# Kernel tuning notes

Hardware: AMD Instinct MI355X
Metric: run time of the kernel (lower is better)

Reference implementation:

```python
import jax, jax.numpy as jnp
import numpy as np

B, IN_LEN, NN, IN_DIM = 32, 28, 2048, 1
E, ND = 256, 256          # embed_dim, node_dim
H = E + ND                # hidden_dim = 512
N_LAYERS = 3
OUT_LEN = 28


def setup_inputs() -> dict:
    key = jax.random.key(0)
    ks = jax.random.split(key, 16)
    x_node = jax.random.normal(ks[0], (B, IN_LEN, NN, IN_DIM), jnp.float32)
    # x_state channels: [0]=cumulative cases, [1]=infected I, [2]=population N
    col0 = jax.random.uniform(ks[1], (B, IN_LEN, NN, 1), jnp.float32) * 100.0
    colI = jax.random.uniform(ks[2], (B, IN_LEN, NN, 1), jnp.float32) * 100.0 + 1.0
    colN = 1e4 * (1.0 + 0.1 * jax.random.uniform(ks[3], (B, IN_LEN, NN, 1), jnp.float32))
    x_state = jnp.concatenate([col0, colI, colN], axis=-1)
    node_emb = jax.random.normal(ks[4], (NN, ND), jnp.float32) * 0.05
    W_ts = jax.random.normal(ks[5], (E, IN_DIM * IN_LEN), jnp.float32) * 0.05
    b_ts = jnp.zeros((E,), jnp.float32)
    enc_W1 = jax.random.normal(ks[6], (N_LAYERS, H, H), jnp.float32) * 0.02
    enc_b1 = jnp.zeros((N_LAYERS, H), jnp.float32)
    enc_W2 = jax.random.normal(ks[7], (N_LAYERS, H, H), jnp.float32) * 0.02
    enc_b2 = jnp.zeros((N_LAYERS, H), jnp.float32)
    Wb = jax.random.normal(ks[8], (1, H), jnp.float32) * 0.05
    bb = jnp.zeros((1,), jnp.float32)
    Wg = jax.random.normal(ks[9], (1, H), jnp.float32) * 0.05
    bg = jnp.zeros((1,), jnp.float32)
    return dict(x_node=x_node, x_state=x_state, node_emb=node_emb,
                W_ts=W_ts, b_ts=b_ts, enc_W1=enc_W1, enc_b1=enc_b1,
                enc_W2=enc_W2, enc_b2=enc_b2, Wb=Wb, bb=bb, Wg=Wg, bg=bg)


def _forward(x_node, x_state, node_emb, W_ts, b_ts,
             enc_W1, enc_b1, enc_W2, enc_b2, Wb, bb, Wg, bg):
    Bn, Lh, Nn, _ = x_node.shape
    # [B,L,N,D] -> [B,N,L*D] (channel = in_dim*in_len for 1x1 conv == linear)
    flat = jnp.transpose(x_node[..., :IN_DIM], (0, 2, 1, 3)).reshape(Bn, Nn, Lh * IN_DIM)
    ts = flat @ W_ts.T + b_ts                                  # [B,N,E]
    h = jnp.concatenate(
        [ts, jnp.broadcast_to(node_emb[None], (Bn,) + node_emb.shape)], axis=-1)  # [B,N,H]
    for l in range(enc_W1.shape[0]):                            # residual MLP encoder
        z = jnp.maximum(h @ enc_W1[l].T + enc_b1[l], 0.0)
        h = h + z @ enc_W2[l].T + enc_b2[l]
    b = jax.nn.sigmoid(h @ Wb.T + bb)                           # [B,N,1] infection rate
    g = jax.nn.sigmoid(h @ Wg.T + bg)                           # [B,N,1] recovery rate

    Npop = x_state[:, -1, :, 2:3]                               # [B,N,1]
    I_hist = x_state[..., 1:2] / g[:, None]                     # [B,L,N,1]
    Iin_hist = jnp.maximum(
        I_hist[:, 1:] - I_hist[:, :-1] + x_state[:, :-1, :, 1:2], 0.0)  # [B,L-1,N,1]
    t1 = jnp.arange(Lh - 1, 0, -1, dtype=jnp.float32)
    w1 = jnp.exp(-g[:, None] * t1[None, :, None, None])         # [B,L-1,N,1]
    I_Tm1 = jnp.sum(w1 * Iin_hist, axis=1)                      # [B,N,1]
    R_Tm1 = Npop - x_state[:, -2, :, 0:1]
    S_Tm1 = Npop - I_Tm1 - R_Tm1
    Iin0 = b * S_Tm1 * I_Tm1 / Npop
    Rin0 = g * I_hist[:, -1, :, 0:1]
    Iin_hist = jnp.concatenate([Iin_hist, Iin0[:, None]], axis=1)  # [B,L,N,1]
    S = S_Tm1 - Iin0
    t2 = jnp.arange(Lh, 0, -1, dtype=jnp.float32)
    w2 = jnp.exp(-g[:, None] * t2[None, :, None, None])
    I = jnp.sum(w2 * Iin_hist, axis=1)                          # [B,N,1]
    R = R_Tm1 + Rin0

    # The torch loop recomputes sum_i exp(-g*(L-i))*Iin_i each step; exact identity:
    # I_new = exp(-g) * (I_old + Iin_new). O(T) scan instead of O(T^2).
    decay = jnp.exp(-g)

    def step(carry, _):
        S, I, R = carry
        Iin = b * S * I / Npop
        S = S - Iin
        Rin = g * I            # uses pre-update I_T, matching torch order
        I = decay * (I + Iin)
        R = R + Rin
        return (S, I, R), Rin

    _, rins = jax.lax.scan(step, (S, I, R), None, length=OUT_LEN)  # [T,B,N,1]
    return jnp.transpose(rins, (1, 0, 2, 3))                       # [B,out_len,N,1]


def reference(x_node, x_state, node_emb, W_ts, b_ts, enc_W1, enc_b1,
              enc_W2, enc_b2, Wb, bb, Wg, bg):
    return _forward(x_node, x_state, node_emb, W_ts, b_ts,
                    enc_W1, enc_b1, enc_W2, enc_b2, Wb, bb, Wg, bg)
```

## Files before the change

kernel.cpp:

```cpp
#include <hip/hip_runtime.h>
#include <hip/hip_bf16.h>
#include <math.h>

#define BATCH 32
#define IN_LEN 28
#define NN 2048
#define E 256
#define H 512
#define N_LAYERS 3
#define OUT_LEN 28
#define M_ROWS (BATCH * NN)

typedef unsigned short u16;
typedef unsigned int   u32;
typedef __attribute__((ext_vector_type(8))) short short8;
typedef __attribute__((ext_vector_type(4))) float f32x4;

#define WAITV(N)  asm volatile("s_waitcnt vmcnt(" #N ")" ::: "memory")
#define BARRIER() __builtin_amdgcn_s_barrier()

__device__ __forceinline__ u16 f2h(float x) {
    union { _Float16 h; u16 u; } v; v.h = (_Float16)x; return v.u;
}
__device__ __forceinline__ float h2f(u16 u) {
    union { _Float16 h; u16 u; } v; v.u = u; return (float)v.h;
}

__device__ __forceinline__ void gload_lds16(const void* g, void* l) {
    __builtin_amdgcn_global_load_lds(
        (const __attribute__((address_space(1))) void*)g,
        (__attribute__((address_space(3))) void*)l, 16, 0, 0);
}

__global__ __launch_bounds__(256)
void k_split2(const float* __restrict__ w1, const float* __restrict__ w2,
              u16* __restrict__ hi, u16* __restrict__ lo, int nW)
{
    int i = blockIdx.x * 256 + threadIdx.x;
    float v = (i < nW) ? w1[i] : w2[i - nW];
    u16 h = f2h(v);
    hi[i] = h;
    lo[i] = f2h(v - h2f(h));
}

__global__ __launch_bounds__(256)
void k_ts(const float* __restrict__ x_node, const float* __restrict__ node_emb,
          const float* __restrict__ W_ts, const float* __restrict__ b_ts,
          u16* __restrict__ hhi, u16* __restrict__ hlo)
{
    __shared__ float xs[IN_LEN][64];
    const int tid = threadIdx.x;
    const int b   = blockIdx.y;
    const int n0  = blockIdx.x * 64;
    const int c   = tid & 127;
    const int sec = tid >> 7;

    for (int idx = tid; idx < IN_LEN * 64; idx += 256) {
        int l = idx >> 6, i = idx & 63;
        xs[l][i] = x_node[((size_t)b * IN_LEN + l) * NN + n0 + i];
    }

    float w0[IN_LEN], w1[IN_LEN];
    float bias0 = 0.f, bias1 = 0.f;
    if (sec == 0) {
        #pragma unroll
        for (int j = 0; j < IN_LEN; j++) {
            w0[j] = W_ts[(2 * c) * IN_LEN + j];
            w1[j] = W_ts[(2 * c + 1) * IN_LEN + j];
        }
        bias0 = b_ts[2 * c];
        bias1 = b_ts[2 * c + 1];
    }
    __syncthreads();

    for (int i = 0; i < 64; i++) {
        size_t row = (size_t)b * NN + n0 + i;
        u32* oh = (u32*)(hhi + row * H);
        u32* ol = (u32*)(hlo + row * H);
        float v0, v1;
        int oc;
        if (sec == 0) {
            v0 = bias0; v1 = bias1;
            #pragma unroll
            for (int j = 0; j < IN_LEN; j++) {
                float x = xs[j][i];
                v0 += x * w0[j];
                v1 += x * w1[j];
            }
            oc = c;
        } else {
            const float2 ev = *(const float2*)&node_emb[(size_t)(n0 + i) * 256 + 2 * c];
            v0 = ev.x; v1 = ev.y;
            oc = 128 + c;
        }
        u16 h0 = f2h(v0), h1 = f2h(v1);
        oh[oc] = (u32)h0 | ((u32)h1 << 16);
        ol[oc] = (u32)f2h(v0 - h2f(h0)) | ((u32)f2h(v1 - h2f(h1)) << 16);
    }
}

__global__ __launch_bounds__(256)
void k_gemm1(const u16* __restrict__ Ahi, const u16* __restrict__ Alo,
             const u16* __restrict__ Whi, const u16* __restrict__ Wlo,
             const float* __restrict__ bias, u16* __restrict__ Z)
{
    __shared__ __align__(16) u16 smem[40960];

    const int tid = threadIdx.x;
    const int ln  = tid & 63;
    const int wv  = tid >> 6;

    const int id   = blockIdx.x;
    const int c    = (id >> 3) & 3;
    const int r    = (id & 7) | ((id >> 5) << 3);
    const int row0 = r * 128;
    const int col0 = c * 128;

    const int rbase = (wv & 1) * 64;
    const int cbase = (wv >> 1) * 64;

    const int lr = ln >> 2;
    const int lc = ln & 3;

    const u16* sgsrc; int sofs; int tb;
    if      (wv == 0) { sgsrc = Ahi; sofs = 0;     tb = row0; }
    else if (wv == 1) { sgsrc = Alo; sofs = 12288; tb = row0; }
    else if (wv == 2) { sgsrc = Whi; sofs = 24576; tb = col0; }
    else              { sgsrc = Wlo; sofs = 32768; tb = col0; }

    auto stage = [&](int p, int kt) {
        u16* dstbuf = smem + sofs + p * 4096;
        #pragma unroll
        for (int i = 0; i < 8; i++) {
            int row = i * 16 + lr;
            int sc  = lc ^ ((row >> 1) & 3);
            gload_lds16(sgsrc + (size_t)(tb + row) * H + kt + sc * 8,
                        dstbuf + i * 512);
        }
    };

    f32x4 acc[4][4];
    #pragma unroll
    for (int m = 0; m < 4; m++)
        #pragma unroll
        for (int n = 0; n < 4; n++) acc[m][n] = (f32x4)(0.f);

    stage(0, 0);
    if (wv < 2) stage(1, 32);

    const int wl = ln & 15;

    for (int t = 0; t < 16; t++) {
        if (wv < 2) { if (t < 15) { WAITV(8); } else { WAITV(0); } }
        else        { WAITV(0); }
        BARRIER();
        if (wv < 2) { if (t + 2 < 16) stage((t + 2) % 3, (t + 2) * 32); }
        else        { if (t + 1 < 16) stage((t + 1) & 1, (t + 1) * 32); }

        const int pa = t % 3, pw = t & 1;
        const u16* bAh = smem + 0     + pa * 4096;
        const u16* bAl = smem + 12288 + pa * 4096;
        const u16* bWh = smem + 24576 + pw * 4096;
        const u16* bWl = smem + 32768 + pw * 4096;

        short8 ahi[4], alo[4], whi[4], wlo[4];
        #pragma unroll
        for (int m = 0; m < 4; m++) {
            int rr = rbase + m * 16 + wl;
            int cc = ((ln >> 4) ^ ((rr >> 1) & 3)) * 8;
            ahi[m] = *(const short8*)&bAh[rr * 32 + cc];
            alo[m] = *(const short8*)&bAl[rr * 32 + cc];
        }
        #pragma unroll
        for (int n = 0; n < 4; n++) {
            int wr = cbase + n * 16 + wl;
            int cc = ((ln >> 4) ^ ((wr >> 1) & 3)) * 8;
            whi[n] = *(const short8*)&bWh[wr * 32 + cc];
            wlo[n] = *(const short8*)&bWl[wr * 32 + cc];
        }
        #pragma unroll
        for (int m = 0; m < 4; m++)
            #pragma unroll
            for (int n = 0; n < 4; n++) {
                acc[m][n] = __builtin_amdgcn_mfma_f32_16x16x32_f16(ahi[m], whi[n], acc[m][n], 0, 0, 0);
                acc[m][n] = __builtin_amdgcn_mfma_f32_16x16x32_f16(ahi[m], wlo[n], acc[m][n], 0, 0, 0);
                acc[m][n] = __builtin_amdgcn_mfma_f32_16x16x32_f16(alo[m], whi[n], acc[m][n], 0, 0, 0);
            }
    }

    __syncthreads();
    u16* zb = smem + wv * 4096;
    float bv[4];
    #pragma unroll
    for (int n = 0; n < 4; n++) bv[n] = bias[col0 + cbase + n * 16 + wl];
    #pragma unroll
    for (int m = 0; m < 4; m++)
        #pragma unroll
        for (int n = 0; n < 4; n++)
            #pragma unroll
            for (int rg = 0; rg < 4; rg++) {
                int row_l = m * 16 + (ln >> 4) * 4 + rg;
                zb[row_l * 64 + n * 16 + wl] =
                    f2h(fmaxf(acc[m][n][rg] + bv[n], 0.f));
            }
    const int cr = ln >> 3;
    const int cc = (ln & 7) * 8;
    #pragma unroll
    for (int p2 = 0; p2 < 8; p2++) {
        int row_l = cr + p2 * 8;
        uint4 v = *(const uint4*)&zb[row_l * 64 + cc];
        *(uint4*)&Z[(size_t)(row0 + rbase + row_l) * H + col0 + cbase + cc] = v;
    }
}

template <int HEAD>
__global__ __launch_bounds__(256)
void k_gemm2(const u16* __restrict__ Z,
             const u16* __restrict__ Whi, const u16* __restrict__ Wlo,
             const float* __restrict__ bias,
             u16* HHi, u16* HLo,
             const float* __restrict__ Wb, const float* __restrict__ Wg,
             float* __restrict__ bSum, float* __restrict__ gSum)
{
    __shared__ __align__(16) u16 smem[32768];

    const int tid = threadIdx.x;
    const int ln  = tid & 63;
    const int wv  = tid >> 6;

    const int id   = blockIdx.x;
    const int c    = (id >> 3) & 3;
    const int r    = (id & 7) | ((id >> 5) << 3);
    const int row0 = r * 128;
    const int col0 = c * 128;

    const int rbase = (wv & 1) * 64;
    const int cbase = (wv >> 1) * 64;

    const int lr = ln >> 2;
    const int lc = ln & 3;

    const u16* sgsrc; int sofs; int tb; int iofs; int niss;
    const bool zw = (wv == 0) || (wv == 3);
    if      (wv == 0) { sgsrc = Z;   sofs = 0;     tb = row0;      iofs = 0;    niss = 4; }
    else if (wv == 3) { sgsrc = Z;   sofs = 0;     tb = row0 + 64; iofs = 2048; niss = 4; }
    else if (wv == 1) { sgsrc = Whi; sofs = 16384; tb = col0;      iofs = 0;    niss = 8; }
    else              { sgsrc = Wlo; sofs = 24576; tb = col0;      iofs = 0;    niss = 8; }

    auto stage = [&](int p, int kt) {
        u16* dstbuf = smem + sofs + p * 4096 + iofs;
        #pragma unroll
        for (int i = 0; i < 8; i++) {
            if (i >= niss) break;
            int row = i * 16 + lr;
            int sc  = lc ^ ((row >> 1) & 3);
            gload_lds16(sgsrc + (size_t)(tb + row) * H + kt + sc * 8,
                        dstbuf + i * 512);
        }
    };

    f32x4 acc[4][4];
    #pragma unroll
    for (int m = 0; m < 4; m++)
        #pragma unroll
        for (int n = 0; n < 4; n++) acc[m][n] = (f32x4)(0.f);

    stage(0, 0);
    if (zw) { stage(1, 32); stage(2, 64); }

    const int wl = ln & 15;

    for (int t = 0; t < 16; t++) {
        if (zw) {
            if      (t < 14) { WAITV(8); }
            else if (t == 14){ WAITV(4); }
            else             { WAITV(0); }
        } else { WAITV(0); }
        BARRIER();
        if (zw) { if (t + 3 < 16) stage((t + 3) & 3, (t + 3) * 32); }
        else    { if (t + 1 < 16) stage((t + 1) & 1, (t + 1) * 32); }

        const int pz = t & 3, pw = t & 1;
        const u16* bZ  = smem + 0     + pz * 4096;
        const u16* bWh = smem + 16384 + pw * 4096;
        const u16* bWl = smem + 24576 + pw * 4096;

        short8 az[4], whi[4], wlo[4];
        #pragma unroll
        for (int m = 0; m < 4; m++) {
            int rr = rbase + m * 16 + wl;
            int cc = ((ln >> 4) ^ ((rr >> 1) & 3)) * 8;
            az[m] = *(const short8*)&bZ[rr * 32 + cc];
        }
        #pragma unroll
        for (int n = 0; n < 4; n++) {
            int wr = cbase + n * 16 + wl;
            int cc = ((ln >> 4) ^ ((wr >> 1) & 3)) * 8;
            whi[n] = *(const short8*)&bWh[wr * 32 + cc];
            wlo[n] = *(const short8*)&bWl[wr * 32 + cc];
        }
        #pragma unroll
        for (int m = 0; m < 4; m++)
            #pragma unroll
            for (int n = 0; n < 4; n++) {
                acc[m][n] = __builtin_amdgcn_mfma_f32_16x16x32_f16(az[m], whi[n], acc[m][n], 0, 0, 0);
                acc[m][n] = __builtin_amdgcn_mfma_f32_16x16x32_f16(az[m], wlo[n], acc[m][n], 0, 0, 0);
            }
    }

    __syncthreads();
    float* fb = (float*)smem + wv * 2048;

    const int cr  = ln >> 3;
    const int ccl = (ln & 7) * 4;
    float pb[8], pg[8];
    if (HEAD) {
        #pragma unroll
        for (int p2 = 0; p2 < 8; p2++) { pb[p2] = 0.f; pg[p2] = 0.f; }
    }

    #pragma unroll
    for (int nh = 0; nh < 2; nh++) {
        #pragma unroll
        for (int m = 0; m < 4; m++)
            #pragma unroll
            for (int j = 0; j < 2; j++)
                #pragma unroll
                for (int rg = 0; rg < 4; rg++) {
                    int row_l = m * 16 + (ln >> 4) * 4 + rg;
                    fb[row_l * 32 + j * 16 + wl] = acc[m][nh * 2 + j][rg];
                }
        const int gc0 = col0 + cbase + nh * 32 + ccl;
        float4 bv = *(const float4*)&bias[gc0];
        float4 hb, hg;
        if (HEAD) {
            hb = *(const float4*)&Wb[gc0];
            hg = *(const float4*)&Wg[gc0];
        }
        #pragma unroll
        for (int p2 = 0; p2 < 8; p2++) {
            int row_l = cr + p2 * 8;
            size_t gidx = (size_t)(row0 + rbase + row_l) * H + gc0;
            uint2 uh = *(const uint2*)(HHi + gidx);
            uint2 ul = *(const uint2*)(HLo + gidx);
            float4 a = *(const float4*)&fb[row_l * 32 + ccl];
            float v0 = a.x + bv.x + h2f((u16)(uh.x & 0xFFFF)) + h2f((u16)(ul.x & 0xFFFF));
            float v1 = a.y + bv.y + h2f((u16)(uh.x >> 16))    + h2f((u16)(ul.x >> 16));
            float v2 = a.z + bv.z + h2f((u16)(uh.y & 0xFFFF)) + h2f((u16)(ul.y & 0xFFFF));
            float v3 = a.w + bv.w + h2f((u16)(uh.y >> 16))    + h2f((u16)(ul.y >> 16));
            if (HEAD) {
                pb[p2] += v0 * hb.x + v1 * hb.y + v2 * hb.z + v3 * hb.w;
                pg[p2] += v0 * hg.x + v1 * hg.y + v2 * hg.z + v3 * hg.w;
            } else {
                u16 h0 = f2h(v0), h1 = f2h(v1), h2 = f2h(v2), h3 = f2h(v3);
                uint2 oh, ol;
                oh.x = (u32)h0 | ((u32)h1 << 16);
                oh.y = (u32)h2 | ((u32)h3 << 16);
                ol.x = (u32)f2h(v0 - h2f(h0)) | ((u32)f2h(v1 - h2f(h1)) << 16);
                ol.y = (u32)f2h(v2 - h2f(h2)) | ((u32)f2h(v3 - h2f(h3)) << 16);
                *(uint2*)(HHi + gidx) = oh;
                *(uint2*)(HLo + gidx) = ol;
            }
        }
    }

    if (HEAD) {
        #pragma unroll
        for (int p2 = 0; p2 < 8; p2++) {
            float sb = pb[p2], sg = pg[p2];
            #pragma unroll
            for (int off = 1; off < 8; off <<= 1) {
                sb += __shfl_xor(sb, off);
                sg += __shfl_xor(sg, off);
            }
            if ((ln & 7) == 0) {
                int grow = row0 + rbase + cr + p2 * 8;
                atomicAdd(&bSum[grow], sb);
                atomicAdd(&gSum[grow], sg);
            }
        }
    }
}

__global__ __launch_bounds__(256)
void k_sir(const float* __restrict__ x_state,
           const float* __restrict__ bSum, const float* __restrict__ gSum,
           const float* __restrict__ bb, const float* __restrict__ bg,
           float* __restrict__ out)
{
    const int row = blockIdx.x * 256 + threadIdx.x;
    const int bb_ = row / NN;
    const int n   = row % NN;

    const float g = 1.f / (1.f + expf(-(gSum[row] + bg[0])));
    const float b = 1.f / (1.f + expf(-(bSum[row] + bb[0])));
    const float d = expf(-g);

    const float* xs = x_state + ((size_t)bb_ * IN_LEN) * (NN * 3) + (size_t)n * 3;

    float x1_prev = xs[1];
    float Ih_prev = x1_prev / g;
    float acc = 0.f;
    #pragma unroll 4
    for (int t = 1; t <= IN_LEN - 1; ++t) {
        float x1 = xs[(size_t)t * (NN * 3) + 1];
        float Ih = x1 / g;
        float Iin = fmaxf(Ih - Ih_prev + x1_prev, 0.f);
        acc = acc * d + Iin;
        Ih_prev = Ih;
        x1_prev = x1;
    }
    float ITm1 = acc * d;
    float Npop = xs[(size_t)(IN_LEN - 1) * (NN * 3) + 2];
    float RTm1 = Npop - xs[(size_t)(IN_LEN - 2) * (NN * 3) + 0];
    float STm1 = Npop - ITm1 - RTm1;
    float Iin0 = b * STm1 * ITm1 / Npop;
    float S = STm1 - Iin0;
    float I = d * (ITm1 + Iin0);

    float* op = out + ((size_t)bb_ * OUT_LEN) * NN + n;
    #pragma unroll 4
    for (int k = 0; k < OUT_LEN; k++) {
        float Iin = b * S * I / Npop;
        S = S - Iin;
        float Rin = g * I;
        I = d * (I + Iin);
        op[(size_t)k * NN] = Rin;
    }
}

extern "C" void kernel_launch(void* const* d_in, const int* in_sizes, int n_in,
                              void* d_out, int out_size, void* d_ws, size_t ws_size,
                              hipStream_t stream)
{
    const float* x_node   = (const float*)d_in[0];
    const float* x_state  = (const float*)d_in[1];
    const float* node_emb = (const float*)d_in[2];
    const float* W_ts     = (const float*)d_in[3];
    const float* b_ts     = (const float*)d_in[4];
    const float* enc_W1   = (const float*)d_in[5];
    const float* enc_b1   = (const float*)d_in[6];
    const float* enc_W2   = (const float*)d_in[7];
    const float* enc_b2   = (const float*)d_in[8];
    const float* Wb       = (const float*)d_in[9];
    const float* bb       = (const float*)d_in[10];
    const float* Wg       = (const float*)d_in[11];
    const float* bg       = (const float*)d_in[12];
    float* out = (float*)d_out;

    u16* hhi   = (u16*)d_ws;
    u16* hlo   = hhi + (size_t)M_ROWS * H;
    u16* wHi   = hlo + (size_t)M_ROWS * H;
    u16* wLo   = wHi + (size_t)6 * H * H;
    float* bSum = (float*)(wLo + (size_t)6 * H * H);
    float* gSum = bSum + M_ROWS;
    u16* z     = (u16*)(gSum + M_ROWS);

    size_t used  = (size_t)((char*)z - (char*)d_ws);
    size_t avail = (ws_size > used) ? ws_size - used : 0;
    long long chunkLL = (long long)(avail / (H * sizeof(u16))) & ~1023LL;
    int chunk = (chunkLL > M_ROWS) ? M_ROWS : (int)chunkLL;
    if (chunk < 1024) chunk = 1024;

    hipMemsetAsync(bSum, 0, 2 * (size_t)M_ROWS * sizeof(float), stream);

    const int nW = N_LAYERS * H * H;
    k_split2<<<2 * nW / 256, 256, 0, stream>>>(enc_W1, enc_W2, wHi, wLo, nW);

    k_ts<<<dim3(NN / 64, BATCH), 256, 0, stream>>>(x_node, node_emb, W_ts, b_ts, hhi, hlo);

    for (int l = 0; l < N_LAYERS; l++) {
        const u16* W1hi = wHi + (size_t)l * H * H;
        const u16* W1lo = wLo + (size_t)l * H * H;
        const u16* W2hi = wHi + (size_t)nW + (size_t)l * H * H;
        const u16* W2lo = wLo + (size_t)nW + (size_t)l * H * H;
        const float* b1 = enc_b1 + (size_t)l * H;
        const float* b2 = enc_b2 + (size_t)l * H;
        for (int r = 0; r < M_ROWS; r += chunk) {
            int rows = (M_ROWS - r < chunk) ? (M_ROWS - r) : chunk;
            u16* hrhi = hhi + (size_t)r * H;
            u16* hrlo = hlo + (size_t)r * H;
            int nblk = (rows / 128) * 4;
            k_gemm1<<<nblk, 256, 0, stream>>>(hrhi, hrlo, W1hi, W1lo, b1, z);
            if (l < N_LAYERS - 1)
                k_gemm2<0><<<nblk, 256, 0, stream>>>(z, W2hi, W2lo, b2, hrhi, hrlo,
                                                     Wb, Wg, bSum + r, gSum + r);
            else
                k_gemm2<1><<<nblk, 256, 0, stream>>>(z, W2hi, W2lo, b2, hrhi, hrlo,
                                                     Wb, Wg, bSum + r, gSum + r);
        }
    }

    k_sir<<<M_ROWS / 256, 256, 0, stream>>>(x_state, bSum, gSum, bb, bg, out);
}
```

Baseline: 766.1 us.

## Use eight waves per GEMM block with split loader roles and hoisted residual loads

Both encoder GEMM kernels now launch 512 threads (8 waves) per 128x128 tile, so each wave owns a 64x32 sub-tile instead of 64x64, and global-to-LDS staging is split across wave pairs. gemm2 moves to triple-buffered weights in a larger LDS allocation, and it prefetches the residual H hi/lo values into registers before the epilogue barrier. The aim is more latency hiding and MFMA issue parallelism within each block. The cost is more LDS per block, fewer resident blocks per CU, and more duplicated A-fragment LDS reads per wave.

```diff
diff --git a/kernel.cpp b/kernel.cpp
--- a/kernel.cpp
+++ b/kernel.cpp
@@ -99,7 +99,7 @@
     }
 }
 
-__global__ __launch_bounds__(256)
+__global__ __launch_bounds__(512)
 void k_gemm1(const u16* __restrict__ Ahi, const u16* __restrict__ Alo,
              const u16* __restrict__ Whi, const u16* __restrict__ Wlo,
              const float* __restrict__ bias, u16* __restrict__ Z)
@@ -117,44 +117,46 @@
     const int col0 = c * 128;
 
     const int rbase = (wv & 1) * 64;
-    const int cbase = (wv >> 1) * 64;
+    const int cbase = (wv >> 1) * 32;
 
     const int lr = ln >> 2;
     const int lc = ln & 3;
 
-    const u16* sgsrc; int sofs; int tb;
-    if      (wv == 0) { sgsrc = Ahi; sofs = 0;     tb = row0; }
-    else if (wv == 1) { sgsrc = Alo; sofs = 12288; tb = row0; }
-    else if (wv == 2) { sgsrc = Whi; sofs = 24576; tb = col0; }
-    else              { sgsrc = Wlo; sofs = 32768; tb = col0; }
+    const int strm = wv >> 1;
+    const int q    = wv & 1;
+    const u16* sgsrc = (strm == 0) ? Ahi : (strm == 1) ? Alo
+                     : (strm == 2) ? Whi : Wlo;
+    const int sofs = (strm == 0) ? 0 : (strm == 1) ? 12288
+                   : (strm == 2) ? 24576 : 32768;
+    const int tb   = (strm < 2) ? row0 : col0;
 
     auto stage = [&](int p, int kt) {
-        u16* dstbuf = smem + sofs + p * 4096;
-        #pragma unroll
-        for (int i = 0; i < 8; i++) {
-            int row = i * 16 + lr;
+        u16* dstbuf = smem + sofs + p * 4096 + q * 2048;
+        #pragma unroll
+        for (int i = 0; i < 4; i++) {
+            int row = q * 64 + i * 16 + lr;
             int sc  = lc ^ ((row >> 1) & 3);
             gload_lds16(sgsrc + (size_t)(tb + row) * H + kt + sc * 8,
                         dstbuf + i * 512);
         }
     };
 
-    f32x4 acc[4][4];
+    f32x4 acc[4][2];
     #pragma unroll
     for (int m = 0; m < 4; m++)
         #pragma unroll
-        for (int n = 0; n < 4; n++) acc[m][n] = (f32x4)(0.f);
+        for (int n = 0; n < 2; n++) acc[m][n] = (f32x4)(0.f);
 
     stage(0, 0);
-    if (wv < 2) stage(1, 32);
+    if (wv < 4) stage(1, 32);
 
     const int wl = ln & 15;
 
     for (int t = 0; t < 16; t++) {
-        if (wv < 2) { if (t < 15) { WAITV(8); } else { WAITV(0); } }
+        if (wv < 4) { if (t < 15) { WAITV(4); } else { WAITV(0); } }
         else        { WAITV(0); }
         BARRIER();
-        if (wv < 2) { if (t + 2 < 16) stage((t + 2) % 3, (t + 2) * 32); }
+        if (wv < 4) { if (t + 2 < 16) stage((t + 2) % 3, (t + 2) * 32); }
         else        { if (t + 1 < 16) stage((t + 1) & 1, (t + 1) * 32); }
 
         const int pa = t % 3, pw = t & 1;
@@ -163,7 +165,7 @@
         const u16* bWh = smem + 24576 + pw * 4096;
         const u16* bWl = smem + 32768 + pw * 4096;
 
-        short8 ahi[4], alo[4], whi[4], wlo[4];
+        short8 ahi[4], alo[4], whi[2], wlo[2];
         #pragma unroll
         for (int m = 0; m < 4; m++) {
             int rr = rbase + m * 16 + wl;
@@ -172,7 +174,7 @@
             alo[m] = *(const short8*)&bAl[rr * 32 + cc];
         }
         #pragma unroll
-        for (int n = 0; n < 4; n++) {
+        for (int n = 0; n < 2; n++) {
             int wr = cbase + n * 16 + wl;
             int cc = ((ln >> 4) ^ ((wr >> 1) & 3)) * 8;
             whi[n] = *(const short8*)&bWh[wr * 32 + cc];
@@ -181,7 +183,7 @@
         #pragma unroll
         for (int m = 0; m < 4; m++)
             #pragma unroll
-            for (int n = 0; n < 4; n++) {
+            for (int n = 0; n < 2; n++) {
                 acc[m][n] = __builtin_amdgcn_mfma_f32_16x16x32_f16(ahi[m], whi[n], acc[m][n], 0, 0, 0);
                 acc[m][n] = __builtin_amdgcn_mfma_f32_16x16x32_f16(ahi[m], wlo[n], acc[m][n], 0, 0, 0);
                 acc[m][n] = __builtin_amdgcn_mfma_f32_16x16x32_f16(alo[m], whi[n], acc[m][n], 0, 0, 0);
@@ -189,32 +191,32 @@
     }
 
     __syncthreads();
-    u16* zb = smem + wv * 4096;
-    float bv[4];
-    #pragma unroll
-    for (int n = 0; n < 4; n++) bv[n] = bias[col0 + cbase + n * 16 + wl];
+    u16* zb = smem + wv * 2048;
+    float bv[2];
+    #pragma unroll
+    for (int n = 0; n < 2; n++) bv[n] = bias[col0 + cbase + n * 16 + wl];
     #pragma unroll
     for (int m = 0; m < 4; m++)
         #pragma unroll
-        for (int n = 0; n < 4; n++)
+        for (int n = 0; n < 2; n++)
             #pragma unroll
             for (int rg = 0; rg < 4; rg++) {
                 int row_l = m * 16 + (ln >> 4) * 4 + rg;
-                zb[row_l * 64 + n * 16 + wl] =
+                zb[row_l * 32 + n * 16 + wl] =
                     f2h(fmaxf(acc[m][n][rg] + bv[n], 0.f));
             }
-    const int cr = ln >> 3;
-    const int cc = (ln & 7) * 8;
-    #pragma unroll
-    for (int p2 = 0; p2 < 8; p2++) {
-        int row_l = cr + p2 * 8;
-        uint4 v = *(const uint4*)&zb[row_l * 64 + cc];
-        *(uint4*)&Z[(size_t)(row0 + rbase + row_l) * H + col0 + cbase + cc] = v;
+    const int cr = ln >> 2;
+    const int cq = (ln & 3) * 8;
+    #pragma unroll
+    for (int p2 = 0; p2 < 4; p2++) {
+        int row_l = cr + p2 * 16;
+        uint4 v = *(const uint4*)&zb[row_l * 32 + cq];
+        *(uint4*)&Z[(size_t)(row0 + rbase + row_l) * H + col0 + cbase + cq] = v;
     }
 }
 
 template <int HEAD>
-__global__ __launch_bounds__(256)
+__global__ __launch_bounds__(512)
 void k_gemm2(const u16* __restrict__ Z,
              const u16* __restrict__ Whi, const u16* __restrict__ Wlo,
              const float* __restrict__ bias,
@@ -222,7 +224,7 @@
              const float* __restrict__ Wb, const float* __restrict__ Wg,
              float* __restrict__ bSum, float* __restrict__ gSum)
 {
-    __shared__ __align__(16) u16 smem[32768];
+    __shared__ __align__(16) u16 smem[40960];
 
     const int tid = threadIdx.x;
     const int ln  = tid & 63;
@@ -235,38 +237,37 @@
     const int col0 = c * 128;
 
     const int rbase = (wv & 1) * 64;
-    const int cbase = (wv >> 1) * 64;
+    const int cbase = (wv >> 1) * 32;
 
     const int lr = ln >> 2;
     const int lc = ln & 3;
 
-    const u16* sgsrc; int sofs; int tb; int iofs; int niss;
-    const bool zw = (wv == 0) || (wv == 3);
-    if      (wv == 0) { sgsrc = Z;   sofs = 0;     tb = row0;      iofs = 0;    niss = 4; }
-    else if (wv == 3) { sgsrc = Z;   sofs = 0;     tb = row0 + 64; iofs = 2048; niss = 4; }
-    else if (wv == 1) { sgsrc = Whi; sofs = 16384; tb = col0;      iofs = 0;    niss = 8; }
-    else              { sgsrc = Wlo; sofs = 24576; tb = col0;      iofs = 0;    niss = 8; }
+    const bool zw = (wv < 2);
+    const bool ww = (wv >= 2) && (wv < 6);
+    const int q = wv & 1;
+    const u16* sgsrc = zw ? Z : (wv < 4 ? Whi : Wlo);
+    const int sofs = zw ? 0 : (wv < 4 ? 16384 : 28672);
+    const int tb   = zw ? row0 : col0;
 
     auto stage = [&](int p, int kt) {
-        u16* dstbuf = smem + sofs + p * 4096 + iofs;
-        #pragma unroll
-        for (int i = 0; i < 8; i++) {
-            if (i >= niss) break;
-            int row = i * 16 + lr;
+        u16* dstbuf = smem + sofs + p * 4096 + q * 2048;
+        #pragma unroll
+        for (int i = 0; i < 4; i++) {
+            int row = q * 64 + i * 16 + lr;
             int sc  = lc ^ ((row >> 1) & 3);
             gload_lds16(sgsrc + (size_t)(tb + row) * H + kt + sc * 8,
                         dstbuf + i * 512);
         }
     };
 
-    f32x4 acc[4][4];
+    f32x4 acc[4][2];
     #pragma unroll
     for (int m = 0; m < 4; m++)
         #pragma unroll
-        for (int n = 0; n < 4; n++) acc[m][n] = (f32x4)(0.f);
-
-    stage(0, 0);
-    if (zw) { stage(1, 32); stage(2, 64); }
+        for (int n = 0; n < 2; n++) acc[m][n] = (f32x4)(0.f);
+
+    if (zw)      { stage(0, 0); stage(1, 32); stage(2, 64); }
+    else if (ww) { stage(0, 0); stage(1, 32); }
 
     const int wl = ln & 15;
 
@@ -275,17 +276,19 @@
             if      (t < 14) { WAITV(8); }
             else if (t == 14){ WAITV(4); }
             else             { WAITV(0); }
-        } else { WAITV(0); }
+        } else if (ww) {
+            if (t < 15) { WAITV(4); } else { WAITV(0); }
+        }
         BARRIER();
-        if (zw) { if (t + 3 < 16) stage((t + 3) & 3, (t + 3) * 32); }
-        else    { if (t + 1 < 16) stage((t + 1) & 1, (t + 1) * 32); }
-
-        const int pz = t & 3, pw = t & 1;
-        const u16* bZ  = smem + 0     + pz * 4096;
-        const u16* bWh = smem + 16384 + pw * 4096;
-        const u16* bWl = smem + 24576 + pw * 4096;
-
-        short8 az[4], whi[4], wlo[4];
+        if (zw)      { if (t + 3 < 16) stage((t + 3) & 3, (t + 3) * 32); }
+        else if (ww) { if (t + 2 < 16) stage((t + 2) % 3, (t + 2) * 32); }
+
+        const int pz = t & 3, pw3 = t % 3;
+        const u16* bZ  = smem + 0     + pz  * 4096;
+        const u16* bWh = smem + 16384 + pw3 * 4096;
+        const u16* bWl = smem + 28672 + pw3 * 4096;
+
+        short8 az[4], whi[2], wlo[2];
         #pragma unroll
         for (int m = 0; m < 4; m++) {
             int rr = rbase + m * 16 + wl;
@@ -293,7 +296,7 @@
             az[m] = *(const short8*)&bZ[rr * 32 + cc];
         }
         #pragma unroll
-        for (int n = 0; n < 4; n++) {
+        for (int n = 0; n < 2; n++) {
             int wr = cbase + n * 16 + wl;
             int cc = ((ln >> 4) ^ ((wr >> 1) & 3)) * 8;
             whi[n] = *(const short8*)&bWh[wr * 32 + cc];
@@ -302,17 +305,33 @@
         #pragma unroll
         for (int m = 0; m < 4; m++)
             #pragma unroll
-            for (int n = 0; n < 4; n++) {
+            for (int n = 0; n < 2; n++) {
                 acc[m][n] = __builtin_amdgcn_mfma_f32_16x16x32_f16(az[m], whi[n], acc[m][n], 0, 0, 0);
                 acc[m][n] = __builtin_amdgcn_mfma_f32_16x16x32_f16(az[m], wlo[n], acc[m][n], 0, 0, 0);
             }
     }
 
-    __syncthreads();
-    float* fb = (float*)smem + wv * 2048;
-
     const int cr  = ln >> 3;
     const int ccl = (ln & 7) * 4;
+    const int gc0 = col0 + cbase + ccl;
+
+    uint2  uhv[8], ulv[8];
+    float4 bvv = *(const float4*)&bias[gc0];
+    float4 hbv, hgv;
+    if (HEAD) {
+        hbv = *(const float4*)&Wb[gc0];
+        hgv = *(const float4*)&Wg[gc0];
+    }
+    #pragma unroll
+    for (int p2 = 0; p2 < 8; p2++) {
+        size_t gidx = (size_t)(row0 + rbase + cr + p2 * 8) * H + gc0;
+        uhv[p2] = *(const uint2*)(HHi + gidx);
+        ulv[p2] = *(const uint2*)(HLo + gidx);
+    }
+
+    BARRIER();
+    float* fb = (float*)smem + wv * 2048;
+
     float pb[8], pg[8];
     if (HEAD) {
         #pragma unroll
@@ -320,47 +339,37 @@
     }
 
     #pragma unroll
-    for (int nh = 0; nh < 2; nh++) {
-        #pragma unroll
-        for (int m = 0; m < 4; m++)
+    for (int m = 0; m < 4; m++)
+        #pragma unroll
+        for (int j = 0; j < 2; j++)
             #pragma unroll
-            for (int j = 0; j < 2; j++)
-                #pragma unroll
-                for (int rg = 0; rg < 4; rg++) {
-                    int row_l = m * 16 + (ln >> 4) * 4 + rg;
-                    fb[row_l * 32 + j * 16 + wl] = acc[m][nh * 2 + j][rg];
-                }
-        const int gc0 = col0 + cbase + nh * 32 + ccl;
-        float4 bv = *(const float4*)&bias[gc0];
-        float4 hb, hg;
+            for (int rg = 0; rg < 4; rg++) {
+                int row_l = m * 16 + (ln >> 4) * 4 + rg;
+                fb[row_l * 32 + j * 16 + wl] = acc[m][j][rg];
+            }
+    #pragma unroll
+    for (int p2 = 0; p2 < 8; p2++) {
+        int row_l = cr + p2 * 8;
+        size_t gidx = (size_t)(row0 + rbase + row_l) * H + gc0;
+        uint2 uh = uhv[p2];
+        uint2 ul = ulv[p2];
+        float4 a = *(const float4*)&fb[row_l * 32 + ccl];
+        float v0 = a.x + bvv.x + h2f((u16)(uh.x & 0xFFFF)) + h2f((u16)(ul.x & 0xFFFF));
+        float v1 = a.y + bvv.y + h2f((u16)(uh.x >> 16))    + h2f((u16)(ul.x >> 16));
+        float v2 = a.z + bvv.z + h2f((u16)(uh.y & 0xFFFF)) + h2f((u16)(ul.y & 0xFFFF));
+        float v3 = a.w + bvv.w + h2f((u16)(uh.y >> 16))    + h2f((u16)(ul.y >> 16));
         if (HEAD) {
-            hb = *(const float4*)&Wb[gc0];
-            hg = *(const float4*)&Wg[gc0];
-        }
-        #pragma unroll
-        for (int p2 = 0; p2 < 8; p2++) {
-            int row_l = cr + p2 * 8;
-            size_t gidx = (size_t)(row0 + rbase + row_l) * H + gc0;
-            uint2 uh = *(const uint2*)(HHi + gidx);
-            uint2 ul = *(const uint2*)(HLo + gidx);
-            float4 a = *(const float4*)&fb[row_l * 32 + ccl];
-            float v0 = a.x + bv.x + h2f((u16)(uh.x & 0xFFFF)) + h2f((u16)(ul.x & 0xFFFF));
-            float v1 = a.y + bv.y + h2f((u16)(uh.x >> 16))    + h2f((u16)(ul.x >> 16));
-            float v2 = a.z + bv.z + h2f((u16)(uh.y & 0xFFFF)) + h2f((u16)(ul.y & 0xFFFF));
-            float v3 = a.w + bv.w + h2f((u16)(uh.y >> 16))    + h2f((u16)(ul.y >> 16));
-            if (HEAD) {
-                pb[p2] += v0 * hb.x + v1 * hb.y + v2 * hb.z + v3 * hb.w;
-                pg[p2] += v0 * hg.x + v1 * hg.y + v2 * hg.z + v3 * hg.w;
-            } else {
-                u16 h0 = f2h(v0), h1 = f2h(v1), h2 = f2h(v2), h3 = f2h(v3);
-                uint2 oh, ol;
-                oh.x = (u32)h0 | ((u32)h1 << 16);
-                oh.y = (u32)h2 | ((u32)h3 << 16);
-                ol.x = (u32)f2h(v0 - h2f(h0)) | ((u32)f2h(v1 - h2f(h1)) << 16);
-                ol.y = (u32)f2h(v2 - h2f(h2)) | ((u32)f2h(v3 - h2f(h3)) << 16);
-                *(uint2*)(HHi + gidx) = oh;
-                *(uint2*)(HLo + gidx) = ol;
-            }
+            pb[p2] += v0 * hbv.x + v1 * hbv.y + v2 * hbv.z + v3 * hbv.w;
+            pg[p2] += v0 * hgv.x + v1 * hgv.y + v2 * hgv.z + v3 * hgv.w;
+        } else {
+            u16 h0 = f2h(v0), h1 = f2h(v1), h2 = f2h(v2), h3 = f2h(v3);
+            uint2 oh, ol;
+            oh.x = (u32)h0 | ((u32)h1 << 16);
+            oh.y = (u32)h2 | ((u32)h3 << 16);
+            ol.x = (u32)f2h(v0 - h2f(h0)) | ((u32)f2h(v1 - h2f(h1)) << 16);
+            ol.y = (u32)f2h(v2 - h2f(h2)) | ((u32)f2h(v3 - h2f(h3)) << 16);
+            *(uint2*)(HHi + gidx) = oh;
+            *(uint2*)(HLo + gidx) = ol;
         }
     }
 
@@ -481,12 +490,12 @@
             u16* hrhi = hhi + (size_t)r * H;
             u16* hrlo = hlo + (size_t)r * H;
             int nblk = (rows / 128) * 4;
-            k_gemm1<<<nblk, 256, 0, stream>>>(hrhi, hrlo, W1hi, W1lo, b1, z);
+            k_gemm1<<<nblk, 512, 0, stream>>>(hrhi, hrlo, W1hi, W1lo, b1, z);
             if (l < N_LAYERS - 1)
-                k_gemm2<0><<<nblk, 256, 0, stream>>>(z, W2hi, W2lo, b2, hrhi, hrlo,
+                k_gemm2<0><<<nblk, 512, 0, stream>>>(z, W2hi, W2lo, b2, hrhi, hrlo,
                                                      Wb, Wg, bSum + r, gSum + r);
             else
-                k_gemm2<1><<<nblk, 256, 0, stream>>>(z, W2hi, W2lo, b2, hrhi, hrlo,
+                k_gemm2<1><<<nblk, 512, 0, stream>>>(z, W2hi, W2lo, b2, hrhi, hrlo,
                                                      Wb, Wg, bSum + r, gSum + r);
         }
     }
```

Result: faster. 700.3 us (-8.6%).
